# Kernel optimization log

Measured on AMD Instinct MI355X. Metric: run time of the kernel, lower is better.

## Reference

```python
import jax, jax.numpy as jnp
import numpy as np

N_NODES = 50000
N_EDGES = 500000
D_FEAT = 128
HIDDEN = 128
EPS = 1e-8


def _lin_init(key, fan_in, fan_out):
    return jax.random.normal(key, (fan_in, fan_out), dtype=jnp.float32) / np.sqrt(fan_in)


def setup_inputs() -> dict:
    key = jax.random.key(0)
    ks = jax.random.split(key, 16)
    h = jax.random.normal(ks[0], (N_NODES, D_FEAT), dtype=jnp.float32)
    coord = jax.random.normal(ks[1], (N_NODES, 3), dtype=jnp.float32)
    vel = jax.random.normal(ks[2], (N_NODES, 3), dtype=jnp.float32)
    edge_index = jax.random.randint(ks[3], (2, N_EDGES), 0, N_NODES, dtype=jnp.int32)
    return {
        "h": h, "coord": coord, "vel": vel, "edge_index": edge_index,
        "W_e1": _lin_init(ks[4], 2 * D_FEAT + 1, HIDDEN), "b_e1": jnp.zeros((HIDDEN,), jnp.float32),
        "W_e2": _lin_init(ks[5], HIDDEN, D_FEAT), "b_e2": jnp.zeros((D_FEAT,), jnp.float32),
        "W_c1": _lin_init(ks[6], D_FEAT, HIDDEN), "b_c1": jnp.zeros((HIDDEN,), jnp.float32),
        "W_c2": _lin_init(ks[7], HIDDEN, 1), "b_c2": jnp.zeros((1,), jnp.float32),
        "W_v1": _lin_init(ks[8], D_FEAT, HIDDEN), "b_v1": jnp.zeros((HIDDEN,), jnp.float32),
        "W_v2": _lin_init(ks[9], HIDDEN, 1), "b_v2": jnp.zeros((1,), jnp.float32),
        "W_n1": _lin_init(ks[10], 2 * D_FEAT, HIDDEN), "b_n1": jnp.zeros((HIDDEN,), jnp.float32),
        "W_n2": _lin_init(ks[11], HIDDEN, D_FEAT), "b_n2": jnp.zeros((D_FEAT,), jnp.float32),
    }


def reference(h, coord, vel, edge_index,
              W_e1, b_e1, W_e2, b_e2,
              W_c1, b_c1, W_c2, b_c2,
              W_v1, b_v1, W_v2, b_v2,
              W_n1, b_n1, W_n2, b_n2):
    act = jax.nn.silu
    r, c = edge_index[0], edge_index[1]
    n = coord.shape[0]

    # coord2radial with normalize=True
    diff = coord[r] - coord[c]                      # [E, 3]
    rad = jnp.sum(diff * diff, axis=-1, keepdims=True)  # [E, 1]
    norm = jnp.sqrt(jax.lax.stop_gradient(rad)) + EPS
    diff = diff / norm

    # edge_op: Linear -> act -> Linear -> act
    edge_in = jnp.concatenate([h[r], h[c], rad], axis=1)  # [E, 2D+1]
    m_ij = act(act(edge_in @ W_e1 + b_e1) @ W_e2 + b_e2)  # [E, D]

    # coord_op: Linear -> act -> Linear (scalar weight per edge)
    weights = act(m_ij @ W_c1 + b_c1) @ W_c2 + b_c2       # [E, 1]
    coors_sum = jax.ops.segment_sum(diff * weights, r, num_segments=n)  # [N, 3]

    # vel_op: Linear -> act -> Linear (scalar per node)
    vel_weights = act(h @ W_v1 + b_v1) @ W_v2 + b_v2      # [N, 1]
    coord_out = coord + coors_sum + vel * vel_weights

    # node aggregation + node_op: Linear -> act -> Linear
    m_i = jax.ops.segment_sum(m_ij, r, num_segments=h.shape[0])  # [N, D]
    agg = jnp.concatenate([h, m_i], axis=1)               # [N, 2D]
    h_out = act(agg @ W_n1 + b_n1) @ W_n2 + b_n2          # [N, D]
    return (h_out, coord_out)
```

## Files before the change

### kernel.cpp

```cpp
#include <hip/hip_runtime.h>
#include <stdint.h>

#define NN 50000
#define NE 500000
#define BLK 256
#define NEB ((NE + 127) / 128)
#define SST 136

#define BARRIER() asm volatile("s_waitcnt lgkmcnt(0)\n\ts_barrier" ::: "memory")

typedef __attribute__((ext_vector_type(8))) short bf16x8;
typedef __attribute__((ext_vector_type(4))) float f32x4;

__device__ __forceinline__ float silu(float x) { return x / (1.0f + __expf(-x)); }
__device__ __forceinline__ float bf2f(unsigned short s) {
    union { unsigned int u; float f; } v; v.u = ((unsigned int)s) << 16; return v.f;
}
__device__ __forceinline__ unsigned short f2bf(float f) {
    union { float f; unsigned int u; } v; v.f = f;
    return (unsigned short)((v.u + 0x7fffu + ((v.u >> 16) & 1u)) >> 16);
}
__device__ __forceinline__ unsigned int pack2(float a, float b) {
    return (unsigned int)f2bf(a) | ((unsigned int)f2bf(b) << 16);
}
__device__ __forceinline__ bf16x8 packf8(const float* p) {
    float4 f0 = *(const float4*)p; float4 f1 = *(const float4*)(p + 4);
    union { bf16x8 v; unsigned int u[4]; } o;
    o.u[0] = pack2(f0.x, f0.y); o.u[1] = pack2(f0.z, f0.w);
    o.u[2] = pack2(f1.x, f1.y); o.u[3] = pack2(f1.z, f1.w);
    return o.v;
}

__global__ void prep_h(const float* __restrict__ h, unsigned short* __restrict__ hb) {
    int i = blockIdx.x * 256 + threadIdx.x;
    if (i < NN * 128 / 4) {
        float4 v = ((const float4*)h)[i];
        uint2 o; o.x = pack2(v.x, v.y); o.y = pack2(v.z, v.w);
        ((uint2*)hb)[i] = o;
    }
}

__global__ void prep_w(const float* __restrict__ We1, const float* __restrict__ We2,
                       const float* __restrict__ Wc1, const float* __restrict__ Wv1,
                       const float* __restrict__ Wn1, const float* __restrict__ Wn2,
                       unsigned short* __restrict__ Wt1, unsigned short* __restrict__ Wt2,
                       unsigned short* __restrict__ Wt3, unsigned short* __restrict__ Wv1t,
                       unsigned short* __restrict__ Wn1t, unsigned short* __restrict__ Wn2t) {
    int i = blockIdx.x * 256 + threadIdx.x;
    if (i < 32768) {
        int j = i >> 8, k = i & 255;
        Wt1[i] = f2bf(We1[k * 128 + j]);
    } else if (i < 49152) {
        int t = i - 32768; int j = t >> 7, ks = t & 127;
        int k0 = (ks & 7) * 16 + (ks >> 3);
        Wt2[t] = f2bf(We2[k0 * 128 + j]);
    } else if (i < 65536) {
        int t = i - 49152; int j = t >> 7, ks = t & 127;
        int k0 = (ks & 7) * 16 + (ks >> 3);
        Wt3[t] = f2bf(Wc1[k0 * 128 + j]);
    } else if (i < 81920) {
        int t = i - 65536; int j = t >> 7, k = t & 127;
        Wv1t[t] = f2bf(Wv1[k * 128 + j]);
    } else if (i < 114688) {
        int t = i - 81920; int j = t >> 8, k = t & 255;
        int ksrc;
        if (k < 128) ksrc = k;
        else { int ks = k - 128; ksrc = 128 + (ks & 7) * 16 + (ks >> 3); }
        Wn1t[t] = f2bf(Wn1[ksrc * 128 + j]);
    } else if (i < 131072) {
        int t = i - 114688; int j = t >> 7, ks = t & 127;
        int k0 = (ks & 7) * 16 + (ks >> 3);
        Wn2t[t] = f2bf(Wn2[k0 * 128 + j]);
    }
}

__global__ void csr_count(const int* __restrict__ eidx, int* __restrict__ deg) {
    int e = blockIdx.x * 256 + threadIdx.x;
    if (e < NE) atomicAdd(&deg[eidx[e]], 1);
}

__global__ void scan_a(const int* __restrict__ deg, int* __restrict__ bsum) {
    __shared__ int s[256];
    int t = threadIdx.x, idx = blockIdx.x * 256 + t;
    s[t] = (idx < NN) ? deg[idx] : 0;
    __syncthreads();
    for (int off = 128; off > 0; off >>= 1) {
        if (t < off) s[t] += s[t + off];
        __syncthreads();
    }
    if (t == 0) bsum[blockIdx.x] = s[0];
}

__global__ void scan_b(int* __restrict__ bsum) {
    __shared__ int s[256];
    int t = threadIdx.x;
    int v = (t < 196) ? bsum[t] : 0;
    s[t] = v;
    __syncthreads();
    for (int off = 1; off < 256; off <<= 1) {
        int x = (t >= off) ? s[t - off] : 0;
        __syncthreads();
        s[t] += x;
        __syncthreads();
    }
    if (t < 196) bsum[t] = s[t] - v;
}

__global__ void scan_c(const int* __restrict__ deg, const int* __restrict__ bsum,
                       int* __restrict__ rowptr) {
    __shared__ int s[256];
    int t = threadIdx.x, idx = blockIdx.x * 256 + t;
    int v = (idx < NN) ? deg[idx] : 0;
    s[t] = v;
    __syncthreads();
    for (int off = 1; off < 256; off <<= 1) {
        int x = (t >= off) ? s[t - off] : 0;
        __syncthreads();
        s[t] += x;
        __syncthreads();
    }
    if (idx < NN) rowptr[idx] = bsum[blockIdx.x] + s[t] - v;
    if (idx == 0) rowptr[NN] = NE;
}

__global__ void csr_fill(const int* __restrict__ eidx, const int* __restrict__ rowptr,
                         int* __restrict__ cursor,
                         int* __restrict__ csr_r, int* __restrict__ csr_c) {
    int e = blockIdx.x * 256 + threadIdx.x;
    if (e < NE) {
        int r = eidx[e], c = eidx[NE + e];
        int slot = rowptr[r] + atomicAdd(&cursor[r], 1);
        csr_r[slot] = r; csr_c[slot] = c;
    }
}

__device__ __forceinline__ void stage256(const unsigned short* __restrict__ W, int halfk,
                                         unsigned short* sW, int tid) {
#pragma unroll
    for (int t = 0; t < 8; ++t) {
        int idx = tid + t * 256; int j = idx >> 4, g = idx & 15;
        *(uint4*)(sW + j * SST + g * 8) = *(const uint4*)(W + (size_t)j * 256 + halfk * 128 + g * 8);
    }
}
__device__ __forceinline__ void stage128(const unsigned short* __restrict__ W,
                                         unsigned short* sW, int tid) {
#pragma unroll
    for (int t = 0; t < 8; ++t) {
        int idx = tid + t * 256; int j = idx >> 4, g = idx & 15;
        *(uint4*)(sW + j * SST + g * 8) = *(const uint4*)(W + (size_t)j * 128 + g * 8);
    }
}
__device__ __forceinline__ void mfma4(const bf16x8 a[2][4], const unsigned short* sW,
                                      int l16, int q, f32x4 acc[2][8]) {
#pragma unroll
    for (int kc = 0; kc < 4; ++kc)
#pragma unroll
        for (int ct = 0; ct < 8; ++ct) {
            bf16x8 b = *(const bf16x8*)(sW + (ct * 16 + l16) * SST + kc * 32 + q * 8);
            acc[0][ct] = __builtin_amdgcn_mfma_f32_16x16x32_bf16(a[0][kc], b, acc[0][ct], 0, 0, 0);
            acc[1][ct] = __builtin_amdgcn_mfma_f32_16x16x32_bf16(a[1][kc], b, acc[1][ct], 0, 0, 0);
        }
}

__global__ __launch_bounds__(BLK, 2) void egcl_edge(
    const float* __restrict__ coord,
    const int* __restrict__ csr_r, const int* __restrict__ csr_c,
    const unsigned short* __restrict__ hb,
    const unsigned short* __restrict__ Wt1,
    const unsigned short* __restrict__ Wt2,
    const unsigned short* __restrict__ Wt3,
    const float* __restrict__ We1,
    const float* __restrict__ be1, const float* __restrict__ be2,
    const float* __restrict__ bc1,
    const float* __restrict__ Wc2, const float* __restrict__ bc2,
    float* __restrict__ m_acc, float* __restrict__ c_sum)
{
    __shared__ __align__(16) unsigned short sAb[128 * SST];
    __shared__ __align__(16) unsigned short sW[128 * SST];
    __shared__ float sRad[128], sDif[128][3];
    __shared__ int sRr[128], sRc[128], sSeg[128];
    __shared__ float sBe1[128], sBe2[128], sBc1[128], sWlast[128], sWc2f[128];

    const int tid = threadIdx.x;
    const int wv = tid >> 6, lane = tid & 63, q = lane >> 4, l16 = lane & 15;
    const int e0 = blockIdx.x * 128;

    if (tid < 128) {
        sBe1[tid] = be1[tid]; sBe2[tid] = be2[tid]; sBc1[tid] = bc1[tid];
        sWlast[tid] = We1[256 * 128 + tid]; sWc2f[tid] = Wc2[tid];
        int s = e0 + tid; int sc = (s < NE) ? s : (NE - 1);
        int r = csr_r[sc], c = csr_c[sc];
        sRr[tid] = r; sRc[tid] = c;
        sSeg[tid] = (s < NE) ? r : -1;
        float dx = coord[r * 3 + 0] - coord[c * 3 + 0];
        float dy = coord[r * 3 + 1] - coord[c * 3 + 1];
        float dz = coord[r * 3 + 2] - coord[c * 3 + 2];
        float rad = fmaf(dx, dx, fmaf(dy, dy, dz * dz));
        float inv = 1.0f / (sqrtf(rad) + 1e-8f);
        sRad[tid] = rad;
        sDif[tid][0] = dx * inv; sDif[tid][1] = dy * inv; sDif[tid][2] = dz * inv;
    }
    stage256(Wt1, 0, sW, tid);
    const float bc2v = bc2[0];
    BARRIER();

    f32x4 acc[2][8];
#pragma unroll
    for (int si = 0; si < 2; ++si)
#pragma unroll
        for (int ct = 0; ct < 8; ++ct) acc[si][ct] = (f32x4){0.f, 0.f, 0.f, 0.f};

    {
        bf16x8 a[2][4];
#pragma unroll
        for (int si = 0; si < 2; ++si) {
            int node = sRr[(wv * 2 + si) * 16 + l16];
#pragma unroll
            for (int kc = 0; kc < 4; ++kc)
                a[si][kc] = *(const bf16x8*)(hb + (size_t)node * 128 + kc * 32 + q * 8);
        }
        mfma4(a, sW, l16, q, acc);
    }
    BARRIER();
    stage256(Wt1, 1, sW, tid);
    BARRIER();
    {
        bf16x8 a[2][4];
#pragma unroll
        for (int si = 0; si < 2; ++si) {
            int node = sRc[(wv * 2 + si) * 16 + l16];
#pragma unroll
            for (int kc = 0; kc < 4; ++kc)
                a[si][kc] = *(const bf16x8*)(hb + (size_t)node * 128 + kc * 32 + q * 8);
        }
        mfma4(a, sW, l16, q, acc);
    }
    BARRIER();

#pragma unroll
    for (int si = 0; si < 2; ++si)
#pragma unroll
        for (int r = 0; r < 4; ++r) {
            int row = (wv * 2 + si) * 16 + q * 4 + r;
            float rad = sRad[row];
            float v[8];
#pragma unroll
            for (int ct = 0; ct < 8; ++ct) {
                int col = ct * 16 + l16;
                v[ct] = silu(acc[si][ct][r] + rad * sWlast[col] + sBe1[col]);
            }
            uint4 pk = make_uint4(pack2(v[0], v[1]), pack2(v[2], v[3]),
                                  pack2(v[4], v[5]), pack2(v[6], v[7]));
            *(uint4*)(sAb + row * SST + l16 * 8) = pk;
        }
    stage128(Wt2, sW, tid);
    BARRIER();

#pragma unroll
    for (int si = 0; si < 2; ++si)
#pragma unroll
        for (int ct = 0; ct < 8; ++ct) acc[si][ct] = (f32x4){0.f, 0.f, 0.f, 0.f};
    {
        bf16x8 a[2][4];
#pragma unroll
        for (int si = 0; si < 2; ++si) {
            int row = (wv * 2 + si) * 16 + l16;
#pragma unroll
            for (int kc = 0; kc < 4; ++kc)
                a[si][kc] = *(const bf16x8*)(sAb + row * SST + kc * 32 + q * 8);
        }
        mfma4(a, sW, l16, q, acc);
    }
    uint4 mu[2][4];
#pragma unroll
    for (int si = 0; si < 2; ++si)
#pragma unroll
        for (int r = 0; r < 4; ++r) {
            float v[8];
#pragma unroll
            for (int ct = 0; ct < 8; ++ct) v[ct] = silu(acc[si][ct][r] + sBe2[ct * 16 + l16]);
            mu[si][r] = make_uint4(pack2(v[0], v[1]), pack2(v[2], v[3]),
                                   pack2(v[4], v[5]), pack2(v[6], v[7]));
        }
    BARRIER();
#pragma unroll
    for (int si = 0; si < 2; ++si)
#pragma unroll
        for (int r = 0; r < 4; ++r) {
            int row = (wv * 2 + si) * 16 + q * 4 + r;
            *(uint4*)(sAb + row * SST + l16 * 8) = mu[si][r];
        }
    stage128(Wt3, sW, tid);
    BARRIER();

#pragma unroll
    for (int si = 0; si < 2; ++si)
#pragma unroll
        for (int ct = 0; ct < 8; ++ct) acc[si][ct] = (f32x4){0.f, 0.f, 0.f, 0.f};
    {
        bf16x8 a[2][4];
#pragma unroll
        for (int si = 0; si < 2; ++si) {
            int row = (wv * 2 + si) * 16 + l16;
#pragma unroll
            for (int kc = 0; kc < 4; ++kc)
                a[si][kc] = *(const bf16x8*)(sAb + row * SST + kc * 32 + q * 8);
        }
        mfma4(a, sW, l16, q, acc);
    }
#pragma unroll
    for (int si = 0; si < 2; ++si) {
        float p[4];
#pragma unroll
        for (int r = 0; r < 4; ++r) {
            float s = 0.f;
#pragma unroll
            for (int ct = 0; ct < 8; ++ct) {
                int col = ct * 16 + l16;
                float t = silu(acc[si][ct][r] + sBc1[col]);
                s = fmaf(t, sWc2f[col], s);
            }
            p[r] = s;
        }
#pragma unroll
        for (int m = 1; m < 16; m <<= 1)
#pragma unroll
            for (int r = 0; r < 4; ++r) p[r] += __shfl_xor(p[r], m, 16);
        if (l16 == 0) {
#pragma unroll
            for (int r = 0; r < 4; ++r) {
                int row = (wv * 2 + si) * 16 + q * 4 + r;
                int rn = sSeg[row];
                if (rn >= 0) {
                    float w = p[r] + bc2v;
                    atomicAdd(&c_sum[(size_t)rn * 3 + 0], sDif[row][0] * w);
                    atomicAdd(&c_sum[(size_t)rn * 3 + 1], sDif[row][1] * w);
                    atomicAdd(&c_sum[(size_t)rn * 3 + 2], sDif[row][2] * w);
                }
            }
        }
    }

    {
        int p = tid & 127, half = tid >> 7;
        int base = half * 64;
        float run = 0.f;
        int cur = sSeg[base];
        bool openL = true;
#pragma unroll 1
        for (int i = 0; i < 64; ++i) {
            int row = base + i;
            int rr = sSeg[row];
            if (rr != cur) {
                if (cur >= 0) {
                    float* dst = &m_acc[(size_t)cur * 128 + p];
                    if (openL) atomicAdd(dst, run);
                    else       *dst = run;
                }
                run = 0.f; cur = rr; openL = false;
            }
            run += bf2f(sAb[row * SST + p]);
        }
        if (cur >= 0) atomicAdd(&m_acc[(size_t)cur * 128 + p], run);
    }
}

__global__ __launch_bounds__(BLK, 3) void egcl_node(
    const unsigned short* __restrict__ hb,
    const float* __restrict__ coord,
    const float* __restrict__ vel,
    const unsigned short* __restrict__ Wv1t, const float* __restrict__ bv1,
    const float* __restrict__ Wv2, const float* __restrict__ bv2,
    const unsigned short* __restrict__ Wn1t, const float* __restrict__ bn1,
    const unsigned short* __restrict__ Wn2t, const float* __restrict__ bn2,
    const float* __restrict__ m_acc, const float* __restrict__ c_sum,
    float* __restrict__ out_h, float* __restrict__ out_c)
{
    __shared__ __align__(16) unsigned short sAb[128 * SST];
    __shared__ float sBv1[128], sWv2f[128], sBn1[128], sBn2[128];

    const int tid = threadIdx.x;
    const int wv = tid >> 6, lane = tid & 63, q = lane >> 4, l16 = lane & 15;
    const int n0 = blockIdx.x * 128;
    int nval = NN - n0; if (nval > 128) nval = 128;

    if (tid < 128) {
        sBv1[tid] = bv1[tid]; sWv2f[tid] = Wv2[tid];
        sBn1[tid] = bn1[tid]; sBn2[tid] = bn2[tid];
    }
    const float bv2v = bv2[0];

    bf16x8 ah[2][4], am[2][4];
#pragma unroll
    for (int si = 0; si < 2; ++si) {
        int row = (wv * 2 + si) * 16 + l16;
        int nn = n0 + row; if (nn >= NN) nn = NN - 1;
#pragma unroll
        for (int kc = 0; kc < 4; ++kc) {
            ah[si][kc] = *(const bf16x8*)(hb + (size_t)nn * 128 + kc * 32 + q * 8);
            am[si][kc] = packf8(m_acc + (size_t)nn * 128 + kc * 32 + q * 8);
        }
    }

    BARRIER();

    f32x4 acc[2][8];
#pragma unroll
    for (int si = 0; si < 2; ++si)
#pragma unroll
        for (int ct = 0; ct < 8; ++ct) acc[si][ct] = (f32x4){0.f, 0.f, 0.f, 0.f};
#pragma unroll
    for (int kc = 0; kc < 4; ++kc)
#pragma unroll
        for (int ct = 0; ct < 8; ++ct) {
            bf16x8 b = *(const bf16x8*)(Wv1t + (size_t)(ct * 16 + l16) * 128 + kc * 32 + q * 8);
            acc[0][ct] = __builtin_amdgcn_mfma_f32_16x16x32_bf16(ah[0][kc], b, acc[0][ct], 0, 0, 0);
            acc[1][ct] = __builtin_amdgcn_mfma_f32_16x16x32_bf16(ah[1][kc], b, acc[1][ct], 0, 0, 0);
        }
#pragma unroll
    for (int si = 0; si < 2; ++si) {
        float p[4];
#pragma unroll
        for (int r = 0; r < 4; ++r) {
            float s = 0.f;
#pragma unroll
            for (int ct = 0; ct < 8; ++ct) {
                int col = ct * 16 + l16;
                float t = silu(acc[si][ct][r] + sBv1[col]);
                s = fmaf(t, sWv2f[col], s);
            }
            p[r] = s;
        }
#pragma unroll
        for (int m = 1; m < 16; m <<= 1)
#pragma unroll
            for (int r = 0; r < 4; ++r) p[r] += __shfl_xor(p[r], m, 16);
        if (l16 == 0) {
#pragma unroll
            for (int r = 0; r < 4; ++r) {
                int row = (wv * 2 + si) * 16 + q * 4 + r;
                int n = n0 + row;
                if (row < nval) {
                    float vw = p[r] + bv2v;
#pragma unroll
                    for (int d = 0; d < 3; ++d) {
                        float cv = coord[(size_t)n * 3 + d] + c_sum[(size_t)n * 3 + d]
                                 + vel[(size_t)n * 3 + d] * vw;
                        out_c[(size_t)n * 3 + d] = cv;
                    }
                }
            }
        }
    }

#pragma unroll
    for (int si = 0; si < 2; ++si)
#pragma unroll
        for (int ct = 0; ct < 8; ++ct) acc[si][ct] = (f32x4){0.f, 0.f, 0.f, 0.f};
#pragma unroll
    for (int kc = 0; kc < 8; ++kc)
#pragma unroll
        for (int ct = 0; ct < 8; ++ct) {
            bf16x8 b = *(const bf16x8*)(Wn1t + (size_t)(ct * 16 + l16) * 256 + kc * 32 + q * 8);
            bf16x8 a0 = (kc < 4) ? ah[0][kc & 3] : am[0][kc & 3];
            bf16x8 a1 = (kc < 4) ? ah[1][kc & 3] : am[1][kc & 3];
            acc[0][ct] = __builtin_amdgcn_mfma_f32_16x16x32_bf16(a0, b, acc[0][ct], 0, 0, 0);
            acc[1][ct] = __builtin_amdgcn_mfma_f32_16x16x32_bf16(a1, b, acc[1][ct], 0, 0, 0);
        }
#pragma unroll
    for (int si = 0; si < 2; ++si)
#pragma unroll
        for (int r = 0; r < 4; ++r) {
            int row = (wv * 2 + si) * 16 + q * 4 + r;
            float v[8];
#pragma unroll
            for (int ct = 0; ct < 8; ++ct) v[ct] = silu(acc[si][ct][r] + sBn1[ct * 16 + l16]);
            uint4 pk = make_uint4(pack2(v[0], v[1]), pack2(v[2], v[3]),
                                  pack2(v[4], v[5]), pack2(v[6], v[7]));
            *(uint4*)(sAb + row * SST + l16 * 8) = pk;
        }

    BARRIER();

#pragma unroll
    for (int si = 0; si < 2; ++si)
#pragma unroll
        for (int ct = 0; ct < 8; ++ct) acc[si][ct] = (f32x4){0.f, 0.f, 0.f, 0.f};
    {
        bf16x8 a[2][4];
#pragma unroll
        for (int si = 0; si < 2; ++si) {
            int row = (wv * 2 + si) * 16 + l16;
#pragma unroll
            for (int kc = 0; kc < 4; ++kc)
                a[si][kc] = *(const bf16x8*)(sAb + row * SST + kc * 32 + q * 8);
        }
#pragma unroll
        for (int kc = 0; kc < 4; ++kc)
#pragma unroll
            for (int ct = 0; ct < 8; ++ct) {
                bf16x8 b = *(const bf16x8*)(Wn2t + (size_t)(ct * 16 + l16) * 128 + kc * 32 + q * 8);
                acc[0][ct] = __builtin_amdgcn_mfma_f32_16x16x32_bf16(a[0][kc], b, acc[0][ct], 0, 0, 0);
                acc[1][ct] = __builtin_amdgcn_mfma_f32_16x16x32_bf16(a[1][kc], b, acc[1][ct], 0, 0, 0);
            }
    }
#pragma unroll
    for (int si = 0; si < 2; ++si)
#pragma unroll
        for (int r = 0; r < 4; ++r) {
            int row = (wv * 2 + si) * 16 + q * 4 + r;
            if (row < nval) {
                float* orow = out_h + (size_t)(n0 + row) * 128;
#pragma unroll
                for (int ct = 0; ct < 8; ++ct)
                    orow[ct * 16 + l16] = acc[si][ct][r] + sBn2[ct * 16 + l16];
            }
        }
}

extern "C" void kernel_launch(void* const* d_in, const int* in_sizes, int n_in,
                              void* d_out, int out_size, void* d_ws, size_t ws_size,
                              hipStream_t stream) {
    const float* h     = (const float*)d_in[0];
    const float* coord = (const float*)d_in[1];
    const float* vel   = (const float*)d_in[2];
    const int*   eidx  = (const int*)d_in[3];
    const float* We1 = (const float*)d_in[4];
    const float* be1 = (const float*)d_in[5];
    const float* We2 = (const float*)d_in[6];
    const float* be2 = (const float*)d_in[7];
    const float* Wc1 = (const float*)d_in[8];
    const float* bc1 = (const float*)d_in[9];
    const float* Wc2 = (const float*)d_in[10];
    const float* bc2 = (const float*)d_in[11];
    const float* Wv1 = (const float*)d_in[12];
    const float* bv1 = (const float*)d_in[13];
    const float* Wv2 = (const float*)d_in[14];
    const float* bv2 = (const float*)d_in[15];
    const float* Wn1 = (const float*)d_in[16];
    const float* bn1 = (const float*)d_in[17];
    const float* Wn2 = (const float*)d_in[18];
    const float* bn2 = (const float*)d_in[19];

    char* ws = (char*)d_ws;
    float* m_acc = (float*)ws;
    float* c_sum = (float*)(ws + 25600000);
    unsigned short* hb   = (unsigned short*)(ws + 26200064);
    unsigned short* Wt1  = (unsigned short*)(ws + 39000064);
    unsigned short* Wt2  = (unsigned short*)(ws + 39065600);
    unsigned short* Wt3  = (unsigned short*)(ws + 39098368);
    unsigned short* Wv1t = (unsigned short*)(ws + 39131136);
    unsigned short* Wn1t = (unsigned short*)(ws + 39163904);
    unsigned short* Wn2t = (unsigned short*)(ws + 39229440);
    int* deg    = (int*)(ws + 39262208);
    int* cursor = (int*)(ws + 39462208);
    int* rowptr = (int*)(ws + 39662208);
    int* bsum   = (int*)(ws + 39862272);
    int* csr_r  = (int*)(ws + 39863296);
    int* csr_c  = (int*)(ws + 41863296);

    hipMemsetAsync(ws, 0, 26200000, stream);
    hipMemsetAsync(ws + 39262208, 0, 400000, stream);

    prep_h<<<6250, 256, 0, stream>>>(h, hb);
    prep_w<<<512, 256, 0, stream>>>(We1, We2, Wc1, Wv1, Wn1, Wn2,
                                    Wt1, Wt2, Wt3, Wv1t, Wn1t, Wn2t);

    csr_count<<<1954, 256, 0, stream>>>(eidx, deg);
    scan_a<<<196, 256, 0, stream>>>(deg, bsum);
    scan_b<<<1, 256, 0, stream>>>(bsum);
    scan_c<<<196, 256, 0, stream>>>(deg, bsum, rowptr);
    csr_fill<<<1954, 256, 0, stream>>>(eidx, rowptr, cursor, csr_r, csr_c);

    egcl_edge<<<NEB, BLK, 0, stream>>>(
        coord, csr_r, csr_c, hb, Wt1, Wt2, Wt3,
        We1, be1, be2, bc1, Wc2, bc2, m_acc, c_sum);

    float* out_h = (float*)d_out;
    float* out_c = out_h + (size_t)NN * 128;
    egcl_node<<<(NN + 127) / 128, BLK, 0, stream>>>(
        hb, coord, vel, Wv1t, bv1, Wv2, bv2, Wn1t, bn1, Wn2t, bn2,
        m_acc, c_sum, out_h, out_c);
}
```

Before: 459.2 us.

## Read MFMA weights directly from global memory and drop block-wide barriers

The edge kernel no longer stages weight tiles into shared memory. MFMA B operands are loaded straight from global (L1/L2-cached) weights, and most block barriers become wave-local waitcnts, since each wave only touches its own rows of sAb. Removing the sW buffer cuts LDS use, which allows launch bounds of 4 blocks per SM. The trade is more global/L2 traffic for weights on every MFMA step and extra register pressure at the higher occupancy target. The segment-reduction loop is also partially unrolled.

```diff
diff --git a/kernel.cpp b/kernel.cpp
--- a/kernel.cpp
+++ b/kernel.cpp
@@ -8,6 +8,7 @@
 #define SST 136
 
 #define BARRIER() asm volatile("s_waitcnt lgkmcnt(0)\n\ts_barrier" ::: "memory")
+#define WAVE_SYNC() asm volatile("s_waitcnt lgkmcnt(0)" ::: "memory")
 
 typedef __attribute__((ext_vector_type(8))) short bf16x8;
 typedef __attribute__((ext_vector_type(4))) float f32x4;
@@ -134,35 +135,20 @@
     }
 }
 
-__device__ __forceinline__ void stage256(const unsigned short* __restrict__ W, int halfk,
-                                         unsigned short* sW, int tid) {
-#pragma unroll
-    for (int t = 0; t < 8; ++t) {
-        int idx = tid + t * 256; int j = idx >> 4, g = idx & 15;
-        *(uint4*)(sW + j * SST + g * 8) = *(const uint4*)(W + (size_t)j * 256 + halfk * 128 + g * 8);
-    }
-}
-__device__ __forceinline__ void stage128(const unsigned short* __restrict__ W,
-                                         unsigned short* sW, int tid) {
-#pragma unroll
-    for (int t = 0; t < 8; ++t) {
-        int idx = tid + t * 256; int j = idx >> 4, g = idx & 15;
-        *(uint4*)(sW + j * SST + g * 8) = *(const uint4*)(W + (size_t)j * 128 + g * 8);
-    }
-}
-__device__ __forceinline__ void mfma4(const bf16x8 a[2][4], const unsigned short* sW,
-                                      int l16, int q, f32x4 acc[2][8]) {
+template<int LDW>
+__device__ __forceinline__ void mfma4g(const bf16x8 a[2][4], const unsigned short* __restrict__ W,
+                                       int l16, int q, f32x4 acc[2][8]) {
 #pragma unroll
     for (int kc = 0; kc < 4; ++kc)
 #pragma unroll
         for (int ct = 0; ct < 8; ++ct) {
-            bf16x8 b = *(const bf16x8*)(sW + (ct * 16 + l16) * SST + kc * 32 + q * 8);
+            bf16x8 b = *(const bf16x8*)(W + (size_t)(ct * 16 + l16) * LDW + kc * 32 + q * 8);
             acc[0][ct] = __builtin_amdgcn_mfma_f32_16x16x32_bf16(a[0][kc], b, acc[0][ct], 0, 0, 0);
             acc[1][ct] = __builtin_amdgcn_mfma_f32_16x16x32_bf16(a[1][kc], b, acc[1][ct], 0, 0, 0);
         }
 }
 
-__global__ __launch_bounds__(BLK, 2) void egcl_edge(
+__global__ __launch_bounds__(BLK, 4) void egcl_edge(
     const float* __restrict__ coord,
     const int* __restrict__ csr_r, const int* __restrict__ csr_c,
     const unsigned short* __restrict__ hb,
@@ -176,9 +162,8 @@
     float* __restrict__ m_acc, float* __restrict__ c_sum)
 {
     __shared__ __align__(16) unsigned short sAb[128 * SST];
-    __shared__ __align__(16) unsigned short sW[128 * SST];
     __shared__ float sRad[128], sDif[128][3];
-    __shared__ int sRr[128], sRc[128], sSeg[128];
+    __shared__ int sRc[128], sSeg[128];
     __shared__ float sBe1[128], sBe2[128], sBc1[128], sWlast[128], sWc2f[128];
 
     const int tid = threadIdx.x;
@@ -190,7 +175,7 @@
         sWlast[tid] = We1[256 * 128 + tid]; sWc2f[tid] = Wc2[tid];
         int s = e0 + tid; int sc = (s < NE) ? s : (NE - 1);
         int r = csr_r[sc], c = csr_c[sc];
-        sRr[tid] = r; sRc[tid] = c;
+        sRc[tid] = c;
         sSeg[tid] = (s < NE) ? r : -1;
         float dx = coord[r * 3 + 0] - coord[c * 3 + 0];
         float dy = coord[r * 3 + 1] - coord[c * 3 + 1];
@@ -200,7 +185,6 @@
         sRad[tid] = rad;
         sDif[tid][0] = dx * inv; sDif[tid][1] = dy * inv; sDif[tid][2] = dz * inv;
     }
-    stage256(Wt1, 0, sW, tid);
     const float bc2v = bc2[0];
     BARRIER();
 
@@ -214,16 +198,14 @@
         bf16x8 a[2][4];
 #pragma unroll
         for (int si = 0; si < 2; ++si) {
-            int node = sRr[(wv * 2 + si) * 16 + l16];
+            int rn = sSeg[(wv * 2 + si) * 16 + l16];
+            int node = (rn < 0) ? 0 : rn;
 #pragma unroll
             for (int kc = 0; kc < 4; ++kc)
                 a[si][kc] = *(const bf16x8*)(hb + (size_t)node * 128 + kc * 32 + q * 8);
         }
-        mfma4(a, sW, l16, q, acc);
-    }
-    BARRIER();
-    stage256(Wt1, 1, sW, tid);
-    BARRIER();
+        mfma4g<256>(a, Wt1, l16, q, acc);
+    }
     {
         bf16x8 a[2][4];
 #pragma unroll
@@ -233,9 +215,8 @@
             for (int kc = 0; kc < 4; ++kc)
                 a[si][kc] = *(const bf16x8*)(hb + (size_t)node * 128 + kc * 32 + q * 8);
         }
-        mfma4(a, sW, l16, q, acc);
-    }
-    BARRIER();
+        mfma4g<256>(a, Wt1 + 128, l16, q, acc);
+    }
 
 #pragma unroll
     for (int si = 0; si < 2; ++si)
@@ -253,8 +234,7 @@
                                   pack2(v[4], v[5]), pack2(v[6], v[7]));
             *(uint4*)(sAb + row * SST + l16 * 8) = pk;
         }
-    stage128(Wt2, sW, tid);
-    BARRIER();
+    WAVE_SYNC();
 
 #pragma unroll
     for (int si = 0; si < 2; ++si)
@@ -269,7 +249,7 @@
             for (int kc = 0; kc < 4; ++kc)
                 a[si][kc] = *(const bf16x8*)(sAb + row * SST + kc * 32 + q * 8);
         }
-        mfma4(a, sW, l16, q, acc);
+        mfma4g<128>(a, Wt2, l16, q, acc);
     }
     uint4 mu[2][4];
 #pragma unroll
@@ -282,7 +262,7 @@
             mu[si][r] = make_uint4(pack2(v[0], v[1]), pack2(v[2], v[3]),
                                    pack2(v[4], v[5]), pack2(v[6], v[7]));
         }
-    BARRIER();
+    WAVE_SYNC();
 #pragma unroll
     for (int si = 0; si < 2; ++si)
 #pragma unroll
@@ -290,8 +270,7 @@
             int row = (wv * 2 + si) * 16 + q * 4 + r;
             *(uint4*)(sAb + row * SST + l16 * 8) = mu[si][r];
         }
-    stage128(Wt3, sW, tid);
-    BARRIER();
+    WAVE_SYNC();
 
 #pragma unroll
     for (int si = 0; si < 2; ++si)
@@ -306,7 +285,7 @@
             for (int kc = 0; kc < 4; ++kc)
                 a[si][kc] = *(const bf16x8*)(sAb + row * SST + kc * 32 + q * 8);
         }
-        mfma4(a, sW, l16, q, acc);
+        mfma4g<128>(a, Wt3, l16, q, acc);
     }
 #pragma unroll
     for (int si = 0; si < 2; ++si) {
@@ -341,13 +320,15 @@
         }
     }
 
+    BARRIER();
+
     {
         int p = tid & 127, half = tid >> 7;
         int base = half * 64;
         float run = 0.f;
         int cur = sSeg[base];
         bool openL = true;
-#pragma unroll 1
+#pragma unroll 4
         for (int i = 0; i < 64; ++i) {
             int row = base + i;
             int rr = sSeg[row];
```

After: 549.0 us. 1.2x slower.

## Prefetch weights into registers and gather both node feature rows up front

Applied to the files above, without the earlier changes.

Weight staging is split into a global-to-register prefetch and a later register-to-LDS write, so each weight matrix load runs during the previous MFMA phase. Edge endpoint indices are now read per lane straight from the CSR arrays, and both h[r] and h[c] rows are gathered into registers before the first barrier, so the second gather's latency no longer stalls the pipeline. This removes the sRr/sRc shared arrays. The cost is much higher register pressure (8 uint4 of weights plus 16 bf16x8 of activations held live), which could cause spills or lower occupancy under launch_bounds(256,2).

```diff
diff --git a/kernel.cpp b/kernel.cpp
--- a/kernel.cpp
+++ b/kernel.cpp
@@ -134,20 +134,27 @@
     }
 }
 
-__device__ __forceinline__ void stage256(const unsigned short* __restrict__ W, int halfk,
-                                         unsigned short* sW, int tid) {
+__device__ __forceinline__ void wpref256(const unsigned short* __restrict__ W, int halfk,
+                                         uint4 w[8], int tid) {
 #pragma unroll
     for (int t = 0; t < 8; ++t) {
         int idx = tid + t * 256; int j = idx >> 4, g = idx & 15;
-        *(uint4*)(sW + j * SST + g * 8) = *(const uint4*)(W + (size_t)j * 256 + halfk * 128 + g * 8);
-    }
-}
-__device__ __forceinline__ void stage128(const unsigned short* __restrict__ W,
-                                         unsigned short* sW, int tid) {
+        w[t] = *(const uint4*)(W + (size_t)j * 256 + halfk * 128 + g * 8);
+    }
+}
+__device__ __forceinline__ void wpref128(const unsigned short* __restrict__ W,
+                                         uint4 w[8], int tid) {
 #pragma unroll
     for (int t = 0; t < 8; ++t) {
         int idx = tid + t * 256; int j = idx >> 4, g = idx & 15;
-        *(uint4*)(sW + j * SST + g * 8) = *(const uint4*)(W + (size_t)j * 128 + g * 8);
+        w[t] = *(const uint4*)(W + (size_t)j * 128 + g * 8);
+    }
+}
+__device__ __forceinline__ void wwrite(const uint4 w[8], unsigned short* sW, int tid) {
+#pragma unroll
+    for (int t = 0; t < 8; ++t) {
+        int idx = tid + t * 256; int j = idx >> 4, g = idx & 15;
+        *(uint4*)(sW + j * SST + g * 8) = w[t];
     }
 }
 __device__ __forceinline__ void mfma4(const bf16x8 a[2][4], const unsigned short* sW,
@@ -178,19 +185,26 @@
     __shared__ __align__(16) unsigned short sAb[128 * SST];
     __shared__ __align__(16) unsigned short sW[128 * SST];
     __shared__ float sRad[128], sDif[128][3];
-    __shared__ int sRr[128], sRc[128], sSeg[128];
+    __shared__ int sSeg[128];
     __shared__ float sBe1[128], sBe2[128], sBc1[128], sWlast[128], sWc2f[128];
 
     const int tid = threadIdx.x;
     const int wv = tid >> 6, lane = tid & 63, q = lane >> 4, l16 = lane & 15;
     const int e0 = blockIdx.x * 128;
+
+    int nr[2], nc[2];
+#pragma unroll
+    for (int si = 0; si < 2; ++si) {
+        int e = e0 + (wv * 2 + si) * 16 + l16;
+        if (e >= NE) e = NE - 1;
+        nr[si] = csr_r[e]; nc[si] = csr_c[e];
+    }
 
     if (tid < 128) {
         sBe1[tid] = be1[tid]; sBe2[tid] = be2[tid]; sBc1[tid] = bc1[tid];
         sWlast[tid] = We1[256 * 128 + tid]; sWc2f[tid] = Wc2[tid];
         int s = e0 + tid; int sc = (s < NE) ? s : (NE - 1);
         int r = csr_r[sc], c = csr_c[sc];
-        sRr[tid] = r; sRc[tid] = c;
         sSeg[tid] = (s < NE) ? r : -1;
         float dx = coord[r * 3 + 0] - coord[c * 3 + 0];
         float dy = coord[r * 3 + 1] - coord[c * 3 + 1];
@@ -200,7 +214,20 @@
         sRad[tid] = rad;
         sDif[tid][0] = dx * inv; sDif[tid][1] = dy * inv; sDif[tid][2] = dz * inv;
     }
-    stage256(Wt1, 0, sW, tid);
+
+    uint4 w[8];
+    wpref256(Wt1, 0, w, tid);
+    wwrite(w, sW, tid);
+
+    bf16x8 ar[2][4], ac[2][4];
+#pragma unroll
+    for (int si = 0; si < 2; ++si)
+#pragma unroll
+        for (int kc = 0; kc < 4; ++kc) {
+            ar[si][kc] = *(const bf16x8*)(hb + (size_t)nr[si] * 128 + kc * 32 + q * 8);
+            ac[si][kc] = *(const bf16x8*)(hb + (size_t)nc[si] * 128 + kc * 32 + q * 8);
+        }
+    wpref256(Wt1, 1, w, tid);
     const float bc2v = bc2[0];
     BARRIER();
 
@@ -210,32 +237,15 @@
 #pragma unroll
         for (int ct = 0; ct < 8; ++ct) acc[si][ct] = (f32x4){0.f, 0.f, 0.f, 0.f};
 
-    {
-        bf16x8 a[2][4];
-#pragma unroll
-        for (int si = 0; si < 2; ++si) {
-            int node = sRr[(wv * 2 + si) * 16 + l16];
-#pragma unroll
-            for (int kc = 0; kc < 4; ++kc)
-                a[si][kc] = *(const bf16x8*)(hb + (size_t)node * 128 + kc * 32 + q * 8);
-        }
-        mfma4(a, sW, l16, q, acc);
-    }
-    BARRIER();
-    stage256(Wt1, 1, sW, tid);
-    BARRIER();
-    {
-        bf16x8 a[2][4];
-#pragma unroll
-        for (int si = 0; si < 2; ++si) {
-            int node = sRc[(wv * 2 + si) * 16 + l16];
-#pragma unroll
-            for (int kc = 0; kc < 4; ++kc)
-                a[si][kc] = *(const bf16x8*)(hb + (size_t)node * 128 + kc * 32 + q * 8);
-        }
-        mfma4(a, sW, l16, q, acc);
-    }
-    BARRIER();
+    mfma4(ar, sW, l16, q, acc);
+    BARRIER();
+    wwrite(w, sW, tid);
+    wpref128(Wt2, w, tid);
+    BARRIER();
+    mfma4(ac, sW, l16, q, acc);
+    BARRIER();
+    wwrite(w, sW, tid);
+    wpref128(Wt3, w, tid);
 
 #pragma unroll
     for (int si = 0; si < 2; ++si)
@@ -253,7 +263,6 @@
                                   pack2(v[4], v[5]), pack2(v[6], v[7]));
             *(uint4*)(sAb + row * SST + l16 * 8) = pk;
         }
-    stage128(Wt2, sW, tid);
     BARRIER();
 
 #pragma unroll
@@ -290,7 +299,7 @@
             int row = (wv * 2 + si) * 16 + q * 4 + r;
             *(uint4*)(sAb + row * SST + l16 * 8) = mu[si][r];
         }
-    stage128(Wt3, sW, tid);
+    wwrite(w, sW, tid);
     BARRIER();
 
 #pragma unroll
@@ -332,10 +341,10 @@
                 int row = (wv * 2 + si) * 16 + q * 4 + r;
                 int rn = sSeg[row];
                 if (rn >= 0) {
-                    float w = p[r] + bc2v;
-                    atomicAdd(&c_sum[(size_t)rn * 3 + 0], sDif[row][0] * w);
-                    atomicAdd(&c_sum[(size_t)rn * 3 + 1], sDif[row][1] * w);
-                    atomicAdd(&c_sum[(size_t)rn * 3 + 2], sDif[row][2] * w);
+                    float wgt = p[r] + bc2v;
+                    atomicAdd(&c_sum[(size_t)rn * 3 + 0], sDif[row][0] * wgt);
+                    atomicAdd(&c_sum[(size_t)rn * 3 + 1], sDif[row][1] * wgt);
+                    atomicAdd(&c_sum[(size_t)rn * 3 + 2], sDif[row][2] * wgt);
                 }
             }
         }
```

After: 457.4 us. Within noise of the previous version (-0.4%).
